# Optimization experiments

Measured on AMD Instinct MI355X. Metric: run time of the kernel, lower is better.

Reference implementation:

```python
import jax, jax.numpy as jnp
import numpy as np
import math

D = 768
H = 12
HD = D // H  # 64


def setup_inputs() -> dict:
    key = jax.random.key(0)
    ks = jax.random.split(key, 8)
    B, S = 32, 127
    desc = jax.random.normal(ks[0], (B, S, D), dtype=jnp.float32)
    nv = jax.random.normal(ks[1], (B, S + 1, D), dtype=jnp.float32)
    def xavier(k, shape):
        fan_in, fan_out = shape[1], shape[0]
        gain = 1.0 / math.sqrt(2.0)
        limit = gain * math.sqrt(6.0 / (fan_in + fan_out))
        return jax.random.uniform(k, shape, jnp.float32, -limit, limit)
    Wq = xavier(ks[2], (D, D)); bq = jnp.zeros((D,), jnp.float32)
    Wk = xavier(ks[3], (D, D)); bk = jnp.zeros((D,), jnp.float32)
    Wv = xavier(ks[4], (D, D)); bv = jnp.zeros((D,), jnp.float32)
    # attn_proj: Linear(3*head_dim, 1)
    Wa = xavier(ks[5], (1, 3 * HD))[0]  # [3*HD]
    ba = jnp.zeros((), jnp.float32)
    return {
        "desc_embeddings": desc,
        "name_value_embeddings": nv,
        "Wq": Wq, "bq": bq, "Wk": Wk, "bk": bk, "Wv": Wv, "bv": bv,
        "Wa": Wa, "ba": ba,
    }


def _forward(desc_embeddings, name_value_embeddings, Wq, bq, Wk, bk, Wv, bv, Wa, ba):
    B, new_seq, _ = name_value_embeddings.shape
    S = new_seq - 1

    # adjacency: var-var all ones, CLS->Var row = 1, Var->CLS col = 0, CLS->CLS = 0
    adj = jnp.zeros((new_seq, new_seq), jnp.float32)
    adj = adj.at[1:, 1:].set(1.0)
    adj = adj.at[0, 1:].set(1.0)
    adj = jnp.broadcast_to(adj, (B, new_seq, new_seq))

    # q,k,v: [B, H, new_seq, HD]
    def proj(W, b):
        y = name_value_embeddings @ W.T + b
        return y.reshape(B, new_seq, H, HD).transpose(0, 2, 1, 3)
    q = proj(Wq, bq); k = proj(Wk, bk); v = proj(Wv, bv)

    # attn_proj weight split: [q_part | k_part | edge_part], each [HD]
    wq_a, wk_a, we_a = Wa[:HD], Wa[HD:2 * HD], Wa[2 * HD:]

    # q/k scalar contributions per (b,h,i) and (b,h,j)
    lq = jnp.einsum('bhid,d->bhi', q, wq_a)  # [B,H,new_seq]
    lk = jnp.einsum('bhjd,d->bhj', k, wk_a)  # [B,H,new_seq]

    # edge_attr[b,i,j] per head h (head slice of concat[node_i_desc, node_j_desc]):
    # edge vector = concat(desc_i, desc_j)[h*HD:(h+1)*HD] viewed as [H, HD] of 2D dims.
    # concat(desc_i, desc_j) has 2D dims -> reshaped to [H, HD] means head h takes
    # slice [h*HD:(h+1)*HD] of the 2D-dim concat. Heads 0..H/2-1 come from desc_i,
    # heads H/2..H-1 come from desc_j. Compute edge dot with we_a accordingly.
    # desc_full[b,t] : [B,S,D]. Build per-head contributions:
    # for h < H//2: edge slice = desc_i[h*HD:(h+1)*HD]  -> depends only on i
    # for h >= H//2: edge slice = desc_j[(h-H//2)*HD:(h-H//2+1)*HD] -> depends only on j
    desc_heads = desc_embeddings.reshape(B, S, H // 2, 2 * HD)  # wrong split; do directly
    # Direct: per head h, slice indices into the 2D concat vector
    dh = desc_embeddings.reshape(B, S, H, HD)  # desc split into H chunks of HD (covers D = H*HD)
    # concat(desc_i,desc_j) reshaped to [H,HD]: heads 0..H/2-1 use dh_i[:, :, h],
    # heads H/2..H-1 use dh_j[:, :, h - H/2]
    e_dot = jnp.einsum('bshd,d->bsh', dh, jnp.broadcast_to(we_a, (HD,)))  # placeholder, recompute per head below
    # per-head edge scalar contribution for var-var edges:
    ei = jnp.einsum('bshd,d->bhs', dh, we_a)  # contribution if head slice comes from desc at position s
    Hh = H // 2
    # var-var logits edge part: for h<Hh depends on i; for h>=Hh depends on j
    le_i = ei[:, :Hh, :]   # [B,Hh,S] depends on i (row)
    le_j = ei[:, Hh:, :]   # [B,Hh,S] depends on j (col)

    # CLS edges: cls_edge_attr = concat(desc, desc) at position t (the var index)
    # row 0 (CLS->var j): edge = concat(desc_j, desc_j) -> head h slice:
    #   h<Hh: dh_j[h]; h>=Hh: dh_j[h-Hh]  -> scalar ei[b,h,j] with h mapped
    e_cls = jnp.concatenate([ei[:, :Hh, :], ei[:, :Hh, :]], axis=1) * 0  # init
    e_cls = jnp.concatenate([le_i, le_i], axis=1)  # [B,H,S]: head h<Hh uses dh[h], h>=Hh uses dh[h-Hh]
    # note ei[:, :Hh] corresponds to dh chunks 0..Hh-1 ; for h>=Hh slice is dh[h-Hh] -> same le_i

    # Assemble full logits [B,H,new_seq,new_seq]
    logits = lq[:, :, :, None] + lk[:, :, None, :]
    # edge contributions (only where adj==1; edge_attr zeroed elsewhere by mask mult)
    edge = jnp.zeros((B, H, new_seq, new_seq), jnp.float32)
    # var-var block [1:,1:]
    ev = jnp.zeros((B, H, S, S), jnp.float32)
    ev = ev + jnp.pad(le_i, ((0, 0), (0, Hh), (0, 0)))[:, :, :, None] * 0  # keep shapes
    ev_i = jnp.concatenate([le_i, jnp.zeros_like(le_j)], axis=1)  # h<Hh: i-dependent
    ev_j = jnp.concatenate([jnp.zeros_like(le_i), le_j], axis=1)  # h>=Hh: j-dependent
    ev = ev_i[:, :, :, None] + ev_j[:, :, None, :]  # [B,H,S,S]
    edge = edge.at[:, :, 1:, 1:].set(ev)
    # CLS row (0, 1:): cls_edge = concat(desc_j,desc_j); j = column var
    edge = edge.at[:, :, 0, 1:].set(e_cls)
    # CLS col (1:, 0): cls_edge = concat(desc_i,desc_i) BUT adj[:,1:,0]=0 so edge_attr
    # multiplied by adj -> zero; also masked out. edge stays 0, but torch zeroes it too.
    # mask edge by adjacency (edge_attr *= adj)
    edge = edge * adj[:, None, :, :]
    logits = logits + edge + ba

    mask = (adj[:, None, :, :] == 0).astype(jnp.float32) * -1e9
    logits = logits + mask
    attn = jax.nn.softmax(logits, axis=-1)  # [B,H,new_seq,new_seq]
    ctx = jnp.einsum('bhij,bhjd->bhid', attn, v)
    basis_outputs = ctx.transpose(0, 2, 1, 3)  # [B,new_seq,H,HD]
    return basis_outputs, attn


def reference(desc_embeddings, name_value_embeddings, Wq, bq, Wk, bk, Wv, bv, Wa, ba):
    return _forward(desc_embeddings, name_value_embeddings, Wq, bq, Wk, bk, Wv, bv, Wa, ba)
```

## Files before the change

kernel.cpp:

```cpp
#include <hip/hip_runtime.h>

#define NB 32
#define NS 128
#define SD 127
#define ND 768
#define NH 12
#define HD 64

__device__ inline float wredSum(float v){
  #pragma unroll
  for (int off=32; off>0; off>>=1) v += __shfl_xor(v, off);
  return v;
}
__device__ inline float wredMax(float v){
  #pragma unroll
  for (int off=32; off>0; off>>=1) v = fmaxf(v, __shfl_xor(v, off));
  return v;
}

__global__ void fold_k(const float* __restrict__ Wk, const float* __restrict__ bk,
                       const float* __restrict__ Wa, float* __restrict__ uk,
                       float* __restrict__ bkdot){
  int t = blockIdx.x*256 + threadIdx.x;
  int h = t / ND, c = t % ND;
  const float* wka = Wa + 64;
  float acc = 0.f;
  #pragma unroll 8
  for (int d=0; d<64; ++d) acc += Wk[(size_t)(h*HD+d)*ND + c] * wka[d];
  uk[h*ND + c] = acc;
  if (blockIdx.x==0 && threadIdx.x < NH){
    int hh = threadIdx.x; float a = 0.f;
    for (int d=0; d<64; ++d) a += bk[hh*HD+d]*wka[d];
    bkdot[hh] = a;
  }
}

__global__ __launch_bounds__(256)
void lk_ei_init(const float* __restrict__ nv, const float* __restrict__ desc,
                const float* __restrict__ uk, const float* __restrict__ bkdot,
                const float* __restrict__ Wa, const float* __restrict__ bv,
                float* __restrict__ lk, float* __restrict__ ei,
                float* __restrict__ ctx){
  __shared__ float sh[ND];
  int blk = blockIdx.x;
  int wave = threadIdx.x >> 6, lane = threadIdx.x & 63;
  if (blk < NB*NS){
    int b = blk >> 7, j = blk & 127;
    const float* row = nv + (size_t)blk * ND;
    for (int c = threadIdx.x; c < ND; c += 256) sh[c] = row[c];
    __syncthreads();
    #pragma unroll
    for (int hh=0; hh<3; ++hh){
      int h = wave*3 + hh;
      float acc = 0.f;
      #pragma unroll
      for (int k=0; k<12; ++k) acc += sh[lane+64*k]*uk[h*ND + lane+64*k];
      acc = wredSum(acc);
      if (lane==0) lk[(b*NH + h)*NS + j] = acc + bkdot[h];
    }
  } else if (blk < NB*NS + NB*SD){
    int bs = blk - NB*NS;
    int b = bs / SD, s = bs % SD;
    float wea = Wa[128 + lane];
    const float* row = desc + (size_t)bs * ND;
    #pragma unroll
    for (int hh=0; hh<3; ++hh){
      int h = wave + hh*4;
      float v = row[h*HD + lane] * wea;
      v = wredSum(v);
      if (lane==0) ei[(b*NH + h)*NS + s] = v;
    }
  } else {
    int idx = (blk - (NB*NS + NB*SD))*256 + threadIdx.x;
    int dq = idx & 15;
    int r  = (idx >> 4) % 24;
    int h  = r >> 1;
    const float* bb = bv + h*HD + dq*4;
    float4 v = { bb[0], bb[1], bb[2], bb[3] };
    ((float4*)ctx)[idx] = v;
  }
}

__global__ __launch_bounds__(256)
void wm_proj(const float* __restrict__ nv, const float* __restrict__ lk,
             const float* __restrict__ ei, const float* __restrict__ Wv,
             float* __restrict__ w, float* __restrict__ ctx){
  int blk = blockIdx.x;
  int cc = blk % 3, bh = blk / 3;
  int b = bh / NH, h = bh % NH;
  __shared__ float w0[NS], w1[NS], m0[256], m1[256];
  int t = threadIdx.x, wave = t >> 6, lane = t & 63;

  if (wave < 2){
    const float* lkrow = lk + bh*NS;
    const float* eirow = ei + (b*NH + (wave==0 ? (h%6) : h))*NS;
    float g = (wave==0) ? 1.f : (h>=6 ? 1.f : 0.f);
    float x0 = (lane>=1) ? lkrow[lane] + g*eirow[lane-1] : -3.0e38f;
    float x1 = lkrow[lane+64] + g*eirow[lane+63];
    float mm = wredMax(fmaxf(x0,x1));
    float e0 = (lane>=1) ? expf(x0-mm) : 0.f;
    float e1 = expf(x1-mm);
    float s  = wredSum(e0+e1);
    float inv = 1.f/s;
    float* wd = wave ? w1 : w0;
    wd[lane]    = e0*inv;
    wd[lane+64] = e1*inv;
  }
  __syncthreads();
  if (cc == 0 && t < NS){
    w[(bh*2 + 0)*NS + t] = w0[t];
    w[(bh*2 + 1)*NS + t] = w1[t];
  }

  const float* nvp = nv + (size_t)(b*NS)*ND + cc*256 + t;
  float a0 = 0.f, a1 = 0.f;
  #pragma unroll 4
  for (int j=1; j<NS; ++j){
    float x = nvp[(size_t)j*ND];
    a0 += w0[j]*x;
    a1 += w1[j]*x;
  }
  m0[t] = a0; m1[t] = a1;
  __syncthreads();

  const float* wvbase = Wv + (size_t)(h*HD)*ND + cc*256;
  #pragma unroll 4
  for (int dd=0; dd<16; ++dd){
    int d = wave*16 + dd;
    const float* wvr = wvbase + (size_t)d*ND;
    float p0 = 0.f, p1 = 0.f;
    #pragma unroll
    for (int k=0; k<4; ++k){
      float wv = wvr[lane + 64*k];
      p0 += wv*m0[lane + 64*k];
      p1 += wv*m1[lane + 64*k];
    }
    p0 = wredSum(p0); p1 = wredSum(p1);
    if (lane==0){
      atomicAdd(&ctx[((size_t)b*24 + h*2    )*HD + d], p0);
      atomicAdd(&ctx[((size_t)b*24 + h*2 + 1)*HD + d], p1);
    }
  }
}

__global__ __launch_bounds__(256)
void write_kernel(const float* __restrict__ ctx, const float* __restrict__ w,
                  float* __restrict__ out){
  int idx = blockIdx.x*256 + threadIdx.x;
  const float4* c4 = (const float4*)ctx;
  const float4* w4 = (const float4*)w;
  float4* o4 = (float4*)out;
  if (idx < 786432){
    int dq = idx & 15;
    int h  = (idx >> 4) % NH;
    int i  = (idx / 192) & 127;
    int b  = idx / 24576;
    o4[idx] = c4[((b*NH + h)*2 + (i != 0))*16 + dq];
  } else {
    int q  = idx - 786432;
    int j4 = q & 31;
    int i  = (q >> 5) & 127;
    int bh = q >> 12;
    o4[idx] = w4[(bh*2 + (i != 0))*32 + j4];
  }
}

extern "C" void kernel_launch(void* const* d_in, const int* in_sizes, int n_in,
                              void* d_out, int out_size, void* d_ws, size_t ws_size,
                              hipStream_t stream) {
  const float* desc = (const float*)d_in[0];
  const float* nv   = (const float*)d_in[1];
  const float* Wk   = (const float*)d_in[4];
  const float* bk   = (const float*)d_in[5];
  const float* Wv   = (const float*)d_in[6];
  const float* bv   = (const float*)d_in[7];
  const float* Wa   = (const float*)d_in[8];
  float* out = (float*)d_out;
  float* ws  = (float*)d_ws;

  float* uk    = ws;
  float* bkdot = ws + 9216;
  float* ei    = ws + 9232;
  float* lkbuf = ws + 58384;
  float* wbuf  = ws + 107536;
  float* ctx   = ws + 205840;

  fold_k      <<<36,   256, 0, stream>>>(Wk, bk, Wa, uk, bkdot);
  lk_ei_init  <<<8208, 256, 0, stream>>>(nv, desc, uk, bkdot, Wa, bv, lkbuf, ei, ctx);
  wm_proj     <<<1152, 256, 0, stream>>>(nv, lkbuf, ei, Wv, wbuf, ctx);
  write_kernel<<<9216, 256, 0, stream>>>(ctx, wbuf, out);
}
```

Measured before the change: 154.9 us.

## Write attention rows directly from wm_proj and parallelize fold_k over more blocks

The attention-matrix output is now written by wm_proj, with each of the three column-chunk blocks writing every third row of the broadcast softmax weights straight from shared memory. This removes the intermediate w buffer and shrinks the final write kernel to only the basis outputs. fold_k is re-tiled to 144 blocks with a split-reduction over d through shared memory, so it no longer runs on just 36 blocks with long serial loops. expf is replaced by __expf, which may slightly change numerics.

```diff
diff --git a/kernel.cpp b/kernel.cpp
--- a/kernel.cpp
+++ b/kernel.cpp
@@ -18,20 +18,26 @@
   return v;
 }
 
-__global__ void fold_k(const float* __restrict__ Wk, const float* __restrict__ bk,
-                       const float* __restrict__ Wa, float* __restrict__ uk,
-                       float* __restrict__ bkdot){
-  int t = blockIdx.x*256 + threadIdx.x;
-  int h = t / ND, c = t % ND;
-  const float* wka = Wa + 64;
+__global__ __launch_bounds__(256)
+void fold_k(const float* __restrict__ Wk, const float* __restrict__ bk,
+            const float* __restrict__ Wa, float* __restrict__ uk,
+            float* __restrict__ bkdot){
+  int blk = blockIdx.x;
+  int h = blk/12, cb = blk%12;
+  int t = threadIdx.x;
+  int c0 = t & 63, dg = t >> 6;
+  const float* base = Wk + (size_t)(h*HD + dg*16)*ND + cb*64 + c0;
   float acc = 0.f;
-  #pragma unroll 8
-  for (int d=0; d<64; ++d) acc += Wk[(size_t)(h*HD+d)*ND + c] * wka[d];
-  uk[h*ND + c] = acc;
-  if (blockIdx.x==0 && threadIdx.x < NH){
-    int hh = threadIdx.x; float a = 0.f;
-    for (int d=0; d<64; ++d) a += bk[hh*HD+d]*wka[d];
-    bkdot[hh] = a;
+  #pragma unroll
+  for (int i=0;i<16;++i) acc += base[(size_t)i*ND] * Wa[64 + dg*16 + i];
+  __shared__ float red[4][64];
+  red[dg][c0] = acc;
+  __syncthreads();
+  if (dg==0) uk[h*ND + cb*64 + c0] = red[0][c0]+red[1][c0]+red[2][c0]+red[3][c0];
+  if (blk==0 && t < NH){
+    float a = 0.f;
+    for (int d=0; d<64; ++d) a += bk[t*HD+d]*Wa[64+d];
+    bkdot[t] = a;
   }
 }
 
@@ -84,7 +90,7 @@
 __global__ __launch_bounds__(256)
 void wm_proj(const float* __restrict__ nv, const float* __restrict__ lk,
              const float* __restrict__ ei, const float* __restrict__ Wv,
-             float* __restrict__ w, float* __restrict__ ctx){
+             float* __restrict__ ctx, float* __restrict__ out){
   int blk = blockIdx.x;
   int cc = blk % 3, bh = blk / 3;
   int b = bh / NH, h = bh % NH;
@@ -98,8 +104,8 @@
     float x0 = (lane>=1) ? lkrow[lane] + g*eirow[lane-1] : -3.0e38f;
     float x1 = lkrow[lane+64] + g*eirow[lane+63];
     float mm = wredMax(fmaxf(x0,x1));
-    float e0 = (lane>=1) ? expf(x0-mm) : 0.f;
-    float e1 = expf(x1-mm);
+    float e0 = (lane>=1) ? __expf(x0-mm) : 0.f;
+    float e1 = __expf(x1-mm);
     float s  = wredSum(e0+e1);
     float inv = 1.f/s;
     float* wd = wave ? w1 : w0;
@@ -107,9 +113,17 @@
     wd[lane+64] = e1*inv;
   }
   __syncthreads();
-  if (cc == 0 && t < NS){
-    w[(bh*2 + 0)*NS + t] = w0[t];
-    w[(bh*2 + 1)*NS + t] = w1[t];
+
+  {
+    float4* ao = (float4*)(out + (size_t)NB*NS*ND + (size_t)bh*NS*NS);
+    int nrows = (NS - cc + 2)/3;
+    for (int idx=t; idx<nrows*32; idx+=256){
+      int rr = idx>>5, q = idx&31;
+      int r = cc + 3*rr;
+      const float* src = (r==0) ? w0 : w1;
+      float4 v = { src[q*4], src[q*4+1], src[q*4+2], src[q*4+3] };
+      ao[r*32+q] = v;
+    }
   }
 
   const float* nvp = nv + (size_t)(b*NS)*ND + cc*256 + t;
@@ -144,25 +158,13 @@
 }
 
 __global__ __launch_bounds__(256)
-void write_kernel(const float* __restrict__ ctx, const float* __restrict__ w,
-                  float* __restrict__ out){
+void basis_kernel(const float* __restrict__ ctx, float* __restrict__ out){
   int idx = blockIdx.x*256 + threadIdx.x;
-  const float4* c4 = (const float4*)ctx;
-  const float4* w4 = (const float4*)w;
-  float4* o4 = (float4*)out;
-  if (idx < 786432){
-    int dq = idx & 15;
-    int h  = (idx >> 4) % NH;
-    int i  = (idx / 192) & 127;
-    int b  = idx / 24576;
-    o4[idx] = c4[((b*NH + h)*2 + (i != 0))*16 + dq];
-  } else {
-    int q  = idx - 786432;
-    int j4 = q & 31;
-    int i  = (q >> 5) & 127;
-    int bh = q >> 12;
-    o4[idx] = w4[(bh*2 + (i != 0))*32 + j4];
-  }
+  int dq = idx & 15;
+  int h  = (idx >> 4) % NH;
+  int i  = (idx / 192) & 127;
+  int b  = idx / 24576;
+  ((float4*)out)[idx] = ((const float4*)ctx)[((b*NH + h)*2 + (i != 0))*16 + dq];
 }
 
 extern "C" void kernel_launch(void* const* d_in, const int* in_sizes, int n_in,
@@ -182,11 +184,10 @@
   float* bkdot = ws + 9216;
   float* ei    = ws + 9232;
   float* lkbuf = ws + 58384;
-  float* wbuf  = ws + 107536;
-  float* ctx   = ws + 205840;
+  float* ctx   = ws + 107536;
 
-  fold_k      <<<36,   256, 0, stream>>>(Wk, bk, Wa, uk, bkdot);
+  fold_k      <<<144,  256, 0, stream>>>(Wk, bk, Wa, uk, bkdot);
   lk_ei_init  <<<8208, 256, 0, stream>>>(nv, desc, uk, bkdot, Wa, bv, lkbuf, ei, ctx);
-  wm_proj     <<<1152, 256, 0, stream>>>(nv, lkbuf, ei, Wv, wbuf, ctx);
-  write_kernel<<<9216, 256, 0, stream>>>(ctx, wbuf, out);
+  wm_proj     <<<1152, 256, 0, stream>>>(nv, lkbuf, ei, Wv, ctx, out);
+  basis_kernel<<<3072, 256, 0, stream>>>(ctx, out);
 }
```

New measurement: 150.8 us. 1.03x faster.
